# Performance work log

Measured on AMD Instinct MI355X. Metric: run time of the kernel, lower is better.

Reference implementation:

```python
import jax, jax.numpy as jnp
import numpy as np

HEADS = 4
EPS_LN = 1e-5
EPS_NORM = 1e-12

def conv1x1(x, w):
    # x: [B,C,T,H,W], w: [O,C] (Conv3d kernel_size=1, no bias)
    return jnp.einsum('oc,bcthw->bothw', w, x)

def dwconv3(x, w):
    # depthwise Conv3d 3x3x3, padding=1; w: [C,1,3,3,3]
    return jax.lax.conv_general_dilated(
        x, w, window_strides=(1, 1, 1), padding='SAME',
        dimension_numbers=('NCDHW', 'OIDHW', 'NCDHW'),
        feature_group_count=x.shape[1])

def layernorm_c(x, w, b):
    # LayerNorm over channel dim (torch LN applied after b c t h w -> b (thw) c)
    m = jnp.mean(x, axis=1, keepdims=True)
    v = jnp.mean(jnp.square(x - m), axis=1, keepdims=True)
    xn = (x - m) * jax.lax.rsqrt(v + EPS_LN)
    return xn * w[None, :, None, None, None] + b[None, :, None, None, None]

def l2norm(x):
    n = jnp.sqrt(jnp.sum(jnp.square(x), axis=-1, keepdims=True))
    return x / jnp.maximum(n, EPS_NORM)

def attention_c(x, qkv_w, qkv_dw_w, proj_w, temperature):
    B, C, T, H, W = x.shape
    qkv = dwconv3(conv1x1(x, qkv_w), qkv_dw_w)  # [B,3C,T,H,W]
    q, k, v = jnp.split(qkv, 3, axis=1)
    def to_heads(a):
        return a.reshape(B, HEADS, C // HEADS, T * H * W)  # b head c (thw)
    q, k, v = to_heads(q), to_heads(k), to_heads(v)
    q = l2norm(q)
    k = l2norm(k)
    # channel attention: [b,h,c,c] score matrix scaled by learnable temperature
    attn = jnp.einsum('bhcn,bhdn->bhcd', q, k) * temperature[None]
    attn = jax.nn.softmax(attn, axis=-1)
    out = jnp.einsum('bhcd,bhdn->bhcn', attn, v)
    out = out.reshape(B, C, T, H, W)
    return conv1x1(out, proj_w)

def feedforward(x, pin_w, ffn_dw_w, pout_w):
    h = conv1x1(x, pin_w)            # [B,2H,T,H,W]
    h = dwconv3(h, ffn_dw_w)
    x1, x2 = jnp.split(h, 2, axis=1)
    g = jax.nn.gelu(x1, approximate=False) * x2
    return conv1x1(g, pout_w)

def setup_inputs() -> dict:
    key = jax.random.key(0)
    ks = jax.random.split(key, 8)
    C, T, H, W = 192, 10, 64, 64
    Hf = int(C * 2.66)  # 510
    s = 0.05
    return {
        'x': jax.random.normal(ks[0], (1, C, T, H, W), jnp.float32),
        'ln1_w': jnp.ones((C,), jnp.float32),
        'ln1_b': jnp.zeros((C,), jnp.float32),
        'qkv_w': jax.random.normal(ks[1], (3 * C, C), jnp.float32) * s,
        'qkv_dw_w': jax.random.normal(ks[2], (3 * C, 1, 3, 3, 3), jnp.float32) * s,
        'proj_w': jax.random.normal(ks[3], (C, C), jnp.float32) * s,
        'temperature': jnp.ones((HEADS, 1, 1), jnp.float32),
        'ln2_w': jnp.ones((C,), jnp.float32),
        'ln2_b': jnp.zeros((C,), jnp.float32),
        'pin_w': jax.random.normal(ks[4], (2 * Hf, C), jnp.float32) * s,
        'ffn_dw_w': jax.random.normal(ks[5], (2 * Hf, 1, 3, 3, 3), jnp.float32) * s,
        'pout_w': jax.random.normal(ks[6], (C, Hf), jnp.float32) * s,
    }

def reference(x, ln1_w, ln1_b, qkv_w, qkv_dw_w, proj_w, temperature,
              ln2_w, ln2_b, pin_w, ffn_dw_w, pout_w):
    y = x + attention_c(layernorm_c(x, ln1_w, ln1_b), qkv_w, qkv_dw_w, proj_w, temperature)
    out = y + feedforward(layernorm_c(y, ln2_w, ln2_b), pin_w, ffn_dw_w, pout_w)
    return out
```

## Files before the change

### kernel.cpp

```cpp
#include <hip/hip_runtime.h>
#include <math.h>

#define NPOS 40960
#define TT 10
#define HH 64
#define WW 64
#define HWP 4096
#define CIN 192
#define C3 576
#define NHEADS 4
#define CHD 48
#define HF 510
#define GNB 80
#define GCHUNK 512

typedef unsigned short u16;
typedef unsigned int   u32;
typedef __bf16 bf16x8 __attribute__((ext_vector_type(8)));
typedef __bf16 bf16x2 __attribute__((ext_vector_type(2)));
typedef float  f32x4  __attribute__((ext_vector_type(4)));
typedef u16    u16x8  __attribute__((ext_vector_type(8)));
typedef u32    u32x4  __attribute__((ext_vector_type(4)));

__device__ __forceinline__ float b2f(u16 u) {
    return __uint_as_float(((unsigned int)u) << 16);
}
__device__ __forceinline__ u16 f2b(float f) {
    unsigned int i = __float_as_uint(f);
    unsigned int r = (i + 0x7FFFu + ((i >> 16) & 1u)) >> 16;
    return (u16)r;
}
__device__ __forceinline__ u16 f2bh(float f) {
    return __builtin_bit_cast(u16, static_cast<__bf16>(f));
}
__device__ __forceinline__ float gelu_exact(float v) {
    return 0.5f * v * (1.0f + erff(v * 0.70710678118654752f));
}
__device__ __forceinline__ float gelu_fast(float v) {
    float z = fabsf(v) * 0.70710678118654752f;
    float d = fmaf(0.3275911f, z, 1.0f);
#if __has_builtin(__builtin_amdgcn_rcpf)
    float t = __builtin_amdgcn_rcpf(d);
#else
    float t = 1.0f / d;
#endif
    float p = fmaf(1.061405429f, t, -1.453152027f);
    p = fmaf(p, t, 1.421413741f);
    p = fmaf(p, t, -0.284496736f);
    p = fmaf(p, t, 0.254829592f);
    p = p * t;
    float e = __expf(-z * z);
    float E = fmaf(-p, e, 1.0f);
    return 0.5f * v * (1.0f + copysignf(E, v));
}

__device__ __forceinline__ float dot2bf(u32 a, u32 b, float c) {
#if __has_builtin(__builtin_amdgcn_fdot2_f32_bf16)
    return __builtin_amdgcn_fdot2_f32_bf16(
        __builtin_bit_cast(bf16x2, a), __builtin_bit_cast(bf16x2, b), c, false);
#else
    float a0 = b2f((u16)(a & 0xffffu)), a1 = b2f((u16)(a >> 16));
    float b0 = b2f((u16)(b & 0xffffu)), b1 = b2f((u16)(b >> 16));
    return fmaf(a1, b1, fmaf(a0, b0, c));
#endif
}
__device__ __forceinline__ u32 alignp(u32 hi, u32 lo) {
#if __has_builtin(__builtin_amdgcn_alignbit)
    return __builtin_amdgcn_alignbit(hi, lo, 16);
#else
    return (lo >> 16) | (hi << 16);
#endif
}

__device__ __forceinline__ u32 dpp_prev(u32 v) {
#if __has_builtin(__builtin_amdgcn_update_dpp)
    return (u32)__builtin_amdgcn_update_dpp(0, (int)v, 0x111, 0xF, 0xF, true);
#else
    return __shfl(v, (threadIdx.x & 63) - 1);
#endif
}
__device__ __forceinline__ u32 dpp_next(u32 v) {
#if __has_builtin(__builtin_amdgcn_update_dpp)
    return (u32)__builtin_amdgcn_update_dpp(0, (int)v, 0x101, 0xF, 0xF, true);
#else
    return __shfl(v, (threadIdx.x & 63) + 1);
#endif
}

#define GLD_LDS16(g, l) __builtin_amdgcn_global_load_lds( \
    (const __attribute__((address_space(1))) void*)(g), \
    (__attribute__((address_space(3))) void*)(l), 16, 0, 0)

#define CVT_N1 (640 * 192)
#define CVT_N2 (1024 * 192)
#define CVT_N3 (256 * 512)
__global__ void cvtw_k(const float* __restrict__ qkv_w, const float* __restrict__ pin_w,
                       const float* __restrict__ pout_w,
                       u16* __restrict__ qkv_wb, u16* __restrict__ pin_wb,
                       u16* __restrict__ pout_wb) {
    int idx = blockIdx.x * 256 + threadIdx.x;
    if (idx < CVT_N1) {
        int r = idx / 192, c = idx % 192;
        qkv_wb[idx] = f2bh(r < 576 ? qkv_w[r * 192 + c] : 0.f);
    } else if (idx < CVT_N1 + CVT_N2) {
        int k = idx - CVT_N1;
        int r = k / 192, c = k % 192;
        pin_wb[k] = f2bh(r < 1020 ? pin_w[r * 192 + c] : 0.f);
    } else if (idx < CVT_N1 + CVT_N2 + CVT_N3) {
        int k = idx - CVT_N1 - CVT_N2;
        int r = k / 512, c = k % 512;
        pout_wb[k] = f2bh((r < 192 && c < 510) ? pout_w[r * 510 + c] : 0.f);
    }
}

template<typename InT>
__global__ __launch_bounds__(256) void lnt_k(const InT* __restrict__ X,
                                             const float* __restrict__ w,
                                             const float* __restrict__ b,
                                             u16* __restrict__ Xt) {
    __shared__ float sm[CIN][65];
    __shared__ float ps[4][64], ps2[4][64];
    __shared__ float smean[64], srstd[64];
    __shared__ float sw[CIN], sb[CIN];
    const int tid = threadIdx.x;
    const int n0 = blockIdx.x * 64;
    if (tid < CIN) { sw[tid] = w[tid]; sb[tid] = b[tid]; }
    if constexpr (sizeof(InT) == 4) {
        #pragma unroll
        for (int i = 0; i < 12; ++i) {
            int e = i * 256 + tid;
            int c = e >> 4, p4 = (e & 15) * 4;
            float4 v = *(const float4*)((const float*)X + (size_t)c * NPOS + n0 + p4);
            sm[c][p4 + 0] = v.x; sm[c][p4 + 1] = v.y;
            sm[c][p4 + 2] = v.z; sm[c][p4 + 3] = v.w;
        }
    } else {
        #pragma unroll
        for (int i = 0; i < 6; ++i) {
            int e = i * 256 + tid;
            int c = e >> 3, p8 = (e & 7) * 8;
            u16x8 v = *(const u16x8*)((const u16*)X + (size_t)c * NPOS + n0 + p8);
            #pragma unroll
            for (int j = 0; j < 8; ++j) sm[c][p8 + j] = b2f(v[j]);
        }
    }
    __syncthreads();
    int g = tid >> 6, nn = tid & 63;
    float s = 0.f, s2 = 0.f;
    for (int c = g * 48; c < g * 48 + 48; ++c) {
        float v = sm[c][nn];
        s += v; s2 += v * v;
    }
    ps[g][nn] = s; ps2[g][nn] = s2;
    __syncthreads();
    if (g == 0) {
        float t = ps[0][nn] + ps[1][nn] + ps[2][nn] + ps[3][nn];
        float t2 = ps2[0][nn] + ps2[1][nn] + ps2[2][nn] + ps2[3][nn];
        float m = t / CIN;
        float var = t2 / CIN - m * m;
        smean[nn] = m;
        srstd[nn] = rsqrtf(var + 1e-5f);
    }
    __syncthreads();
    #pragma unroll
    for (int i = 0; i < 6; ++i) {
        int e = i * 256 + tid;
        int nl = e / 24, cg = e % 24;
        int c0 = cg * 8;
        float m = smean[nl], rs_ = srstd[nl];
        u16x8 o;
        #pragma unroll
        for (int j = 0; j < 8; ++j) {
            float v = (sm[c0 + j][nl] - m) * rs_ * sw[c0 + j] + sb[c0 + j];
            o[j] = f2bh(v);
        }
        *(u16x8*)(Xt + (size_t)(n0 + nl) * CIN + c0) = o;
    }
}

__global__ __launch_bounds__(256) void transpose_pad_k(const u16* __restrict__ src,
                                                       u16* __restrict__ dst,
                                                       int CS, int CD) {
    __shared__ float sm[64][65];
    const int tid = threadIdx.x;
    const int n0 = blockIdx.x * 64;
    const int cb = blockIdx.y * 64;
    #pragma unroll
    for (int i = 0; i < 2; ++i) {
        int e = i * 256 + tid;
        int cl = e >> 3, nn8 = (e & 7) * 8;
        int c = cb + cl;
        if (c < CS) {
            u16x8 v = *(const u16x8*)(src + (size_t)c * NPOS + n0 + nn8);
            #pragma unroll
            for (int j = 0; j < 8; ++j) sm[cl][nn8 + j] = b2f(v[j]);
        } else {
            #pragma unroll
            for (int j = 0; j < 8; ++j) sm[cl][nn8 + j] = 0.f;
        }
    }
    __syncthreads();
    #pragma unroll
    for (int i = 0; i < 2; ++i) {
        int e = i * 256 + tid;
        int nl = e >> 3, c0 = (e & 7) * 8;
        u16x8 o;
        #pragma unroll
        for (int j = 0; j < 8; ++j) o[j] = f2bh(sm[c0 + j][nl]);
        *(u16x8*)(dst + (size_t)(n0 + nl) * CD + cb + c0) = o;
    }
}

template<int KP, typename OutT, typename ResT, bool RESID>
__global__ __launch_bounds__(256) void gemm_mfma_k(
    const u16* __restrict__ A, const u16* __restrict__ Bt, int O,
    const ResT* __restrict__ resid, OutT* __restrict__ outp)
{
    constexpr int NT = KP / 32;
    __shared__ u16 As[2][128 * 32];
    __shared__ u16 Bs[2][128 * 32];
    const int tid  = threadIdx.x;
    const int lane = tid & 63;
    const int wv   = tid >> 6;
    const int lo = lane & 15, hi = lane >> 4;
    const int m_blk = blockIdx.y * 128;
    const int n_blk = blockIdx.x * 128;

    int bb0 = (0 * 4 + wv) * 1024 + lane * 16;
    int bb1 = (1 * 4 + wv) * 1024 + lane * 16;
    const int r0 = bb0 >> 6, c80 = (bb0 >> 4) & 3;
    const int r1 = bb1 >> 6, c81 = (bb1 >> 4) & 3;

    auto stage = [&](int buf, int k0) {
        GLD_LDS16(A  + (size_t)(m_blk + r0) * KP + k0 + c80 * 8, (char*)&As[buf][0] + (0 * 4 + wv) * 1024);
        GLD_LDS16(A  + (size_t)(m_blk + r1) * KP + k0 + c81 * 8, (char*)&As[buf][0] + (1 * 4 + wv) * 1024);
        GLD_LDS16(Bt + (size_t)(n_blk + r0) * KP + k0 + c80 * 8, (char*)&Bs[buf][0] + (0 * 4 + wv) * 1024);
        GLD_LDS16(Bt + (size_t)(n_blk + r1) * KP + k0 + c81 * 8, (char*)&Bs[buf][0] + (1 * 4 + wv) * 1024);
    };

    f32x4 acc[4][4];
    const f32x4 zero = {0.f, 0.f, 0.f, 0.f};
    #pragma unroll
    for (int mt = 0; mt < 4; ++mt)
        #pragma unroll
        for (int nt = 0; nt < 4; ++nt) acc[mt][nt] = zero;

    stage(0, 0);
    __syncthreads();

    #pragma unroll
    for (int t = 0; t < NT; ++t) {
        if (t + 1 < NT) stage((t + 1) & 1, (t + 1) * 32);
        const u16* Ab = &As[t & 1][0] + (wv & 1) * 64 * 32;
        const u16* Bb = &Bs[t & 1][0] + (wv >> 1) * 64 * 32;
        bf16x8 a[4], b[4];
        #pragma unroll
        for (int q = 0; q < 4; ++q) {
            a[q] = *(const bf16x8*)(Ab + (q * 16 + lo) * 32 + hi * 8);
            b[q] = *(const bf16x8*)(Bb + (q * 16 + lo) * 32 + hi * 8);
        }
        #pragma unroll
        for (int mt = 0; mt < 4; ++mt)
            #pragma unroll
            for (int nt = 0; nt < 4; ++nt)
                acc[mt][nt] = __builtin_amdgcn_mfma_f32_16x16x32_bf16(
                    a[mt], b[nt], acc[mt][nt], 0, 0, 0);
        __syncthreads();
    }

    const int m_base = m_blk + (wv & 1) * 64;
    const int n_base = n_blk + (wv >> 1) * 64;
    #pragma unroll
    for (int mt = 0; mt < 4; ++mt) {
        #pragma unroll
        for (int r = 0; r < 4; ++r) {
            int m = m_base + mt * 16 + hi * 4 + r;
            if (m < O) {
                size_t rowoff = (size_t)m * NPOS;
                #pragma unroll
                for (int nt = 0; nt < 4; ++nt) {
                    int n = n_base + nt * 16 + lo;
                    float v = acc[mt][nt][r];
                    if (RESID) {
                        if constexpr (sizeof(ResT) == 2) v += b2f(((const u16*)resid)[rowoff + n]);
                        else                             v += ((const float*)resid)[rowoff + n];
                    }
                    if constexpr (sizeof(OutT) == 2) outp[rowoff + n] = (OutT)f2bh(v);
                    else                             outp[rowoff + n] = (OutT)v;
                }
            }
        }
    }
}

__global__ __launch_bounds__(256) void dwconv_k(const u16* __restrict__ in,
                                                u16* __restrict__ outp,
                                                const float* __restrict__ wgt,
                                                float* __restrict__ nrm2)
{
    __shared__ float red[256];
    const int lane = threadIdx.x & 63;
    const int wv   = threadIdx.x >> 6;
    const int c    = blockIdx.x >> 1;
    const int hb   = blockIdx.x & 1;
    const int h    = hb * 32 + wv * 8 + (lane >> 3);
    const int w0c  = (lane & 7) * 8;
    const bool wl0 = (lane & 7) == 0;
    const bool wl7 = (lane & 7) == 7;
    const bool hup = (h > 0), hdn = (h < HH - 1);
    u32 W01[9], W2h[9];
    {
        const float* wc = wgt + c * 27;
        #pragma unroll
        for (int i = 0; i < 9; ++i) {
            float a = wc[i * 3 + 0], b = wc[i * 3 + 1], d = wc[i * 3 + 2];
            W01[i] = (u32)f2b(a) | ((u32)f2b(b) << 16);
            W2h[i] = ((u32)f2b(d)) << 16;
        }
    }
    const u16* base = in   + (size_t)c * (TT * HWP);
    u16*       ob   = outp + (size_t)c * (TT * HWP);

    u32x4 zv = {0u, 0u, 0u, 0u};
    u32x4 ld[3][3];
    auto issue = [&](int ph, int ts) {
        const u16* rp = base + (size_t)ts * HWP + h * WW + w0c;
        ld[ph][0] = hup ? *(const u32x4*)(rp - WW) : zv;
        ld[ph][1] = *(const u32x4*)(rp);
        ld[ph][2] = hdn ? *(const u32x4*)(rp + WW) : zv;
    };

    float acc[3][8];
    #pragma unroll
    for (int o_ = 0; o_ < 3; ++o_)
        #pragma unroll
        for (int j = 0; j < 8; ++j) acc[o_][j] = 0.f;
    float sq = 0.f;

    issue(0, 0);
    issue(1, 1);
    #pragma unroll
    for (int ts = 0; ts < TT; ++ts) {
        const int cb = ts % 3;
        if (ts + 2 < TT) issue((ts + 2) % 3, ts + 2);
        #pragma unroll
        for (int dh = 0; dh < 3; ++dh) {
            u32 P0 = ld[cb][dh][0], P1 = ld[cb][dh][1];
            u32 P2 = ld[cb][dh][2], P3 = ld[cb][dh][3];
            u32 Pm = dpp_prev(P3); Pm = wl0 ? 0u : Pm;
            u32 Pp = dpp_next(P0); Pp = wl7 ? 0u : Pp;
            u32 S0 = alignp(P0, Pm), S1 = alignp(P1, P0);
            u32 S2 = alignp(P2, P1), S3 = alignp(P3, P2);
            u32 S4 = alignp(Pp, P3);
            #pragma unroll
            for (int tp = 0; tp < 3; ++tp) {
                int o_;
                if (tp == 2) { if (ts < 1) continue; o_ = (ts - 1) % 3; }
                else if (tp == 1) { o_ = ts % 3; }
                else { if (ts + 1 >= TT) continue; o_ = (ts + 1) % 3; }
                const u32 wA = W01[tp * 3 + dh], wB = W2h[tp * 3 + dh];
                float* ap = acc[o_];
                ap[0] = dot2bf(S0, wA, ap[0]); ap[0] = dot2bf(P0, wB, ap[0]);
                ap[1] = dot2bf(P0, wA, ap[1]); ap[1] = dot2bf(S1, wB, ap[1]);
                ap[2] = dot2bf(S1, wA, ap[2]); ap[2] = dot2bf(P1, wB, ap[2]);
                ap[3] = dot2bf(P1, wA, ap[3]); ap[3] = dot2bf(S2, wB, ap[3]);
                ap[4] = dot2bf(S2, wA, ap[4]); ap[4] = dot2bf(P2, wB, ap[4]);
                ap[5] = dot2bf(P2, wA, ap[5]); ap[5] = dot2bf(S3, wB, ap[5]);
                ap[6] = dot2bf(S3, wA, ap[6]); ap[6] = dot2bf(P3, wB, ap[6]);
                ap[7] = dot2bf(P3, wA, ap[7]); ap[7] = dot2bf(S4, wB, ap[7]);
            }
        }
        if (ts >= 1) {
            const int o_ = (ts - 1) % 3;
            u16x8 o;
            #pragma unroll
            for (int j = 0; j < 8; ++j) {
                float v = acc[o_][j];
                sq = fmaf(v, v, sq);
                o[j] = f2bh(v);
            }
            *(u16x8*)(ob + (size_t)(ts - 1) * HWP + h * WW + w0c) = o;
            #pragma unroll
            for (int j = 0; j < 8; ++j) acc[o_][j] = 0.f;
        }
    }
    {
        const int o_ = (TT - 1) % 3;
        u16x8 o;
        #pragma unroll
        for (int j = 0; j < 8; ++j) {
            float v = acc[o_][j];
            sq = fmaf(v, v, sq);
            o[j] = f2bh(v);
        }
        *(u16x8*)(ob + (size_t)(TT - 1) * HWP + h * WW + w0c) = o;
    }
    if (nrm2) {
        red[threadIdx.x] = sq;
        __syncthreads();
        for (int off = 128; off > 0; off >>= 1) {
            if (threadIdx.x < off) red[threadIdx.x] += red[threadIdx.x + off];
            __syncthreads();
        }
        if (threadIdx.x == 0) nrm2[c * 2 + hb] = red[0];
    }
}

__global__ __launch_bounds__(256) void dwconv_glu2_k(const u16* __restrict__ in,
                                                     u16* __restrict__ gout,
                                                     const float* __restrict__ wgt)
{
    __shared__ float gbuf[2][16][66];
    const int tid  = threadIdx.x;
    const int lane = tid & 63;
    const int wv   = tid >> 6;
    const int ch   = wv >> 1;
    const int wvc  = wv & 1;
    const int cpr  = blockIdx.x >> 2;
    const int hb   = blockIdx.x & 3;
    const int hr   = wvc * 8 + (lane >> 3);
    const int h    = hb * 16 + hr;
    const int w0c  = (lane & 7) * 8;
    const bool wl0 = (lane & 7) == 0;
    const bool wl7 = (lane & 7) == 7;
    const bool hup = (h > 0), hdn = (h < HH - 1);

    const int cc = __builtin_amdgcn_readfirstlane(cpr + ch * HF);
    u32 W01[9], W2h[9];
    {
        const float* wc = wgt + (size_t)cc * 27;
        #pragma unroll
        for (int i = 0; i < 9; ++i) {
            float a = wc[i * 3 + 0], b = wc[i * 3 + 1], d = wc[i * 3 + 2];
            W01[i] = (u32)f2b(a) | ((u32)f2b(b) << 16);
            W2h[i] = ((u32)f2b(d)) << 16;
        }
    }
    const u16* base = in + (size_t)cc * (TT * HWP);
    u16* ob = gout + (size_t)cpr * (TT * HWP);

    u32x4 zv = {0u, 0u, 0u, 0u};
    u32x4 ld[3][3];
    auto issue = [&](int ph, int ts) {
        const u16* rp = base + (size_t)ts * HWP + h * WW + w0c;
        ld[ph][0] = hup ? *(const u32x4*)(rp - WW) : zv;
        ld[ph][1] = *(const u32x4*)(rp);
        ld[ph][2] = hdn ? *(const u32x4*)(rp + WW) : zv;
    };

    float acc[3][8];
    #pragma unroll
    for (int o_ = 0; o_ < 3; ++o_)
        #pragma unroll
        for (int j = 0; j < 8; ++j) acc[o_][j] = 0.f;

    auto emit = [&](int ots) {
        const int o_ = ots % 3;
        const int bf = ots & 1;
        if (ch == 0) {
            #pragma unroll
            for (int j = 0; j < 8; ++j) {
                float a = acc[o_][j];
                gbuf[bf][hr][w0c + j] = (j < 4) ? gelu_fast(a) : a;
            }
        }
        __syncthreads();
        if (ch == 1) {
            u16x8 o;
            #pragma unroll
            for (int j = 0; j < 8; ++j) {
                float v = gbuf[bf][hr][w0c + j];
                float g = (j < 4) ? v : gelu_fast(v);
                o[j] = f2bh(g * acc[o_][j]);
            }
            *(u16x8*)(ob + (size_t)ots * HWP + h * WW + w0c) = o;
        }
        #pragma unroll
        for (int j = 0; j < 8; ++j) acc[o_][j] = 0.f;
    };

    issue(0, 0);
    issue(1, 1);
    #pragma unroll
    for (int ts = 0; ts < TT; ++ts) {
        const int cb = ts % 3;
        if (ts + 2 < TT) issue((ts + 2) % 3, ts + 2);
        #pragma unroll
        for (int dh = 0; dh < 3; ++dh) {
            u32 P0 = ld[cb][dh][0], P1 = ld[cb][dh][1];
            u32 P2 = ld[cb][dh][2], P3 = ld[cb][dh][3];
            u32 Pm = dpp_prev(P3); Pm = wl0 ? 0u : Pm;
            u32 Pp = dpp_next(P0); Pp = wl7 ? 0u : Pp;
            u32 S0 = alignp(P0, Pm), S1 = alignp(P1, P0);
            u32 S2 = alignp(P2, P1), S3 = alignp(P3, P2);
            u32 S4 = alignp(Pp, P3);
            #pragma unroll
            for (int tp = 0; tp < 3; ++tp) {
                int o_;
                if (tp == 2) { if (ts < 1) continue; o_ = (ts - 1) % 3; }
                else if (tp == 1) { o_ = ts % 3; }
                else { if (ts + 1 >= TT) continue; o_ = (ts + 1) % 3; }
                const u32 wA = W01[tp * 3 + dh], wB = W2h[tp * 3 + dh];
                float* ap = acc[o_];
                ap[0] = dot2bf(S0, wA, ap[0]); ap[0] = dot2bf(P0, wB, ap[0]);
                ap[1] = dot2bf(P0, wA, ap[1]); ap[1] = dot2bf(S1, wB, ap[1]);
                ap[2] = dot2bf(S1, wA, ap[2]); ap[2] = dot2bf(P1, wB, ap[2]);
                ap[3] = dot2bf(P1, wA, ap[3]); ap[3] = dot2bf(S2, wB, ap[3]);
                ap[4] = dot2bf(S2, wA, ap[4]); ap[4] = dot2bf(P2, wB, ap[4]);
                ap[5] = dot2bf(P2, wA, ap[5]); ap[5] = dot2bf(S3, wB, ap[5]);
                ap[6] = dot2bf(S3, wA, ap[6]); ap[6] = dot2bf(P3, wB, ap[6]);
                ap[7] = dot2bf(P3, wA, ap[7]); ap[7] = dot2bf(S4, wB, ap[7]);
            }
        }
        if (ts >= 1) emit(ts - 1);
    }
    emit(TT - 1);
}

__global__ __launch_bounds__(64) void gram_k(const u16* __restrict__ qkv,
                                             float* __restrict__ part) {
    const int h  = blockIdx.x / GNB;
    const int nb = blockIdx.x % GNB;
    const int lane = threadIdx.x;
    const int lo = lane & 15, hi = lane >> 4;
    const u16* qp = qkv + (size_t)(h * CHD) * NPOS + (size_t)nb * GCHUNK + hi * 8;
    const u16* kp = qkv + (size_t)(CIN + h * CHD) * NPOS + (size_t)nb * GCHUNK + hi * 8;
    f32x4 acc[3][3];
    const f32x4 zero = {0.f, 0.f, 0.f, 0.f};
    #pragma unroll
    for (int mt = 0; mt < 3; ++mt)
        #pragma unroll
        for (int nt = 0; nt < 3; ++nt) acc[mt][nt] = zero;
    #pragma unroll
    for (int ks = 0; ks < GCHUNK; ks += 32) {
        bf16x8 a[3], b[3];
        #pragma unroll
        for (int t = 0; t < 3; ++t) {
            a[t] = *(const bf16x8*)(qp + (size_t)(t * 16 + lo) * NPOS + ks);
            b[t] = *(const bf16x8*)(kp + (size_t)(t * 16 + lo) * NPOS + ks);
        }
        #pragma unroll
        for (int mt = 0; mt < 3; ++mt)
            #pragma unroll
            for (int nt = 0; nt < 3; ++nt)
                acc[mt][nt] = __builtin_amdgcn_mfma_f32_16x16x32_bf16(
                    a[mt], b[nt], acc[mt][nt], 0, 0, 0);
    }
    float* pp = part + (size_t)blockIdx.x * 2304;
    #pragma unroll
    for (int mt = 0; mt < 3; ++mt)
        #pragma unroll
        for (int nt = 0; nt < 3; ++nt)
            #pragma unroll
            for (int r = 0; r < 4; ++r)
                pp[(mt * 16 + hi * 4 + r) * 48 + nt * 16 + lo] = acc[mt][nt][r];
}

__global__ __launch_bounds__(64) void gram_softmax_k(const float* __restrict__ part,
                                                     const float* __restrict__ norm2p,
                                                     const float* __restrict__ temp,
                                                     float* __restrict__ attn) {
    const int row = blockIdx.x;
    const int h = row / CHD, r = row % CHD;
    const int d = threadIdx.x;
    float s = 0.f;
    if (d < CHD) {
        const float* pp = part + (size_t)h * GNB * 2304 + r * 48 + d;
        for (int nb = 0; nb < GNB; ++nb) s += pp[(size_t)nb * 2304];
    }
    float v = -1e30f;
    if (d < CHD) {
        float qn = fmaxf(sqrtf(norm2p[2 * row] + norm2p[2 * row + 1]), 1e-12f);
        int kc = CIN + h * CHD + d;
        float kn = fmaxf(sqrtf(norm2p[2 * kc] + norm2p[2 * kc + 1]), 1e-12f);
        v = temp[h] * s / (qn * kn);
    }
    float mx = v;
    #pragma unroll
    for (int o = 32; o > 0; o >>= 1) mx = fmaxf(mx, __shfl_xor(mx, o));
    float e = (d < CHD) ? expf(v - mx) : 0.f;
    float se = e;
    #pragma unroll
    for (int o = 32; o > 0; o >>= 1) se += __shfl_xor(se, o);
    if (d < CHD) attn[row * CHD + d] = e / se;
}

__global__ void mmat_k(const float* __restrict__ proj_w, const float* __restrict__ attn,
                       u16* __restrict__ Mb) {
    int idx = blockIdx.x * blockDim.x + threadIdx.x;
    if (idx >= 256 * CIN) return;
    int o = idx / CIN, j = idx % CIN;
    float s = 0.f;
    if (o < CIN) {
        int h = j / CHD, d = j % CHD;
        for (int c = 0; c < CHD; ++c)
            s += proj_w[o * CIN + h * CHD + c] * attn[(h * CHD + c) * CHD + d];
    }
    Mb[idx] = f2bh(s);
}

extern "C" void kernel_launch(void* const* d_in, const int* in_sizes, int n_in,
                              void* d_out, int out_size, void* d_ws, size_t ws_size,
                              hipStream_t stream) {
    const float* x       = (const float*)d_in[0];
    const float* ln1w    = (const float*)d_in[1];
    const float* ln1b    = (const float*)d_in[2];
    const float* qkv_w   = (const float*)d_in[3];
    const float* qkv_dw  = (const float*)d_in[4];
    const float* proj_w  = (const float*)d_in[5];
    const float* temp    = (const float*)d_in[6];
    const float* ln2w    = (const float*)d_in[7];
    const float* ln2b    = (const float*)d_in[8];
    const float* pin_w   = (const float*)d_in[9];
    const float* ffn_dw  = (const float*)d_in[10];
    const float* pout_w  = (const float*)d_in[11];
    float* out = (float*)d_out;

    char* wsb = (char*)d_ws;
    size_t off = 0;
    auto alloc = [&](size_t bytes) {
        void* p = wsb + off; off += (bytes + 255) & ~(size_t)255; return p;
    };
    float* norm2p  = (float*)alloc(C3 * 2 * 4);
    float* attn    = (float*)alloc(NHEADS * 2304 * 4);
    float* part    = (float*)alloc((size_t)NHEADS * GNB * 2304 * 4);
    u16*   qkv_wb  = (u16*)alloc((size_t)640 * 192 * 2);
    u16*   pin_wb  = (u16*)alloc((size_t)1024 * 192 * 2);
    u16*   pout_wb = (u16*)alloc((size_t)256 * 512 * 2);
    u16*   M_b     = (u16*)alloc((size_t)256 * 192 * 2);
    u16*   xn1_t   = (u16*)alloc((size_t)NPOS * 192 * 2);
    u16*   yn2_t   = (u16*)alloc((size_t)NPOS * 192 * 2);
    u16*   ybuf    = (u16*)alloc((size_t)CIN * NPOS * 2);
    u16*   regionA = (u16*)alloc((size_t)1024 * NPOS * 2);
    u16*   regionB = (u16*)alloc((size_t)1024 * NPOS * 2);
    u16* qkv_raw  = regionA;
    u16* qkv_conv = regionB;
    u16* h_raw    = regionA;
    u16* g510     = regionB;
    u16* gt       = regionA;
    u16* vt       = xn1_t;

    cvtw_k<<<(CVT_N1 + CVT_N2 + CVT_N3 + 255) / 256, 256, 0, stream>>>(
        qkv_w, pin_w, pout_w, qkv_wb, pin_wb, pout_wb);
    lnt_k<float><<<NPOS / 64, 256, 0, stream>>>(x, ln1w, ln1b, xn1_t);
    gemm_mfma_k<192, u16, float, false><<<dim3(NPOS / 128, 5), 256, 0, stream>>>(
        qkv_wb, xn1_t, C3, nullptr, qkv_raw);
    dwconv_k<<<C3 * 2, 256, 0, stream>>>(qkv_raw, qkv_conv, qkv_dw, norm2p);
    gram_k<<<NHEADS * GNB, 64, 0, stream>>>(qkv_conv, part);
    gram_softmax_k<<<192, 64, 0, stream>>>(part, norm2p, temp, attn);
    mmat_k<<<(256 * CIN + 255) / 256, 256, 0, stream>>>(proj_w, attn, M_b);
    transpose_pad_k<<<dim3(NPOS / 64, 3), 256, 0, stream>>>(
        qkv_conv + (size_t)384 * NPOS, vt, 192, 192);
    gemm_mfma_k<192, u16, float, true><<<dim3(NPOS / 128, 2), 256, 0, stream>>>(
        M_b, vt, CIN, x, ybuf);
    lnt_k<u16><<<NPOS / 64, 256, 0, stream>>>(ybuf, ln2w, ln2b, yn2_t);
    gemm_mfma_k<192, u16, float, false><<<dim3(NPOS / 128, 8), 256, 0, stream>>>(
        pin_wb, yn2_t, 1024, nullptr, h_raw);
    dwconv_glu2_k<<<HF * 4, 256, 0, stream>>>(h_raw, g510, ffn_dw);
    transpose_pad_k<<<dim3(NPOS / 64, 8), 256, 0, stream>>>(g510, gt, HF, 512);
    gemm_mfma_k<512, float, u16, true><<<dim3(NPOS / 128, 2), 256, 0, stream>>>(
        pout_wb, gt, CIN, ybuf, out);
}
```

Measured before the change: 232.8 us.

## Compute both GLU channels per thread to remove LDS exchange and barriers

New measurement: 233.6 us. Within noise of the previous version (+0.4%).

```diff
diff --git a/kernel.cpp b/kernel.cpp
--- a/kernel.cpp
+++ b/kernel.cpp
@@ -20,7 +20,9 @@
 typedef __bf16 bf16x2 __attribute__((ext_vector_type(2)));
 typedef float  f32x4  __attribute__((ext_vector_type(4)));
 typedef u16    u16x8  __attribute__((ext_vector_type(8)));
+typedef u16    u16x4  __attribute__((ext_vector_type(4)));
 typedef u32    u32x4  __attribute__((ext_vector_type(4)));
+typedef u32    u32x2  __attribute__((ext_vector_type(2)));
 
 __device__ __forceinline__ float b2f(u16 u) {
     return __uint_as_float(((unsigned int)u) << 16);
@@ -32,9 +34,6 @@
 }
 __device__ __forceinline__ u16 f2bh(float f) {
     return __builtin_bit_cast(u16, static_cast<__bf16>(f));
-}
-__device__ __forceinline__ float gelu_exact(float v) {
-    return 0.5f * v * (1.0f + erff(v * 0.70710678118654752f));
 }
 __device__ __forceinline__ float gelu_fast(float v) {
     float z = fabsf(v) * 0.70710678118654752f;
@@ -76,15 +75,27 @@
 #if __has_builtin(__builtin_amdgcn_update_dpp)
     return (u32)__builtin_amdgcn_update_dpp(0, (int)v, 0x111, 0xF, 0xF, true);
 #else
-    return __shfl(v, (threadIdx.x & 63) - 1);
+    int l = (int)(threadIdx.x & 63);
+    u32 r = __shfl(v, l - 1);
+    return ((l & 15) == 0) ? 0u : r;
 #endif
 }
 __device__ __forceinline__ u32 dpp_next(u32 v) {
 #if __has_builtin(__builtin_amdgcn_update_dpp)
     return (u32)__builtin_amdgcn_update_dpp(0, (int)v, 0x101, 0xF, 0xF, true);
 #else
-    return __shfl(v, (threadIdx.x & 63) + 1);
+    int l = (int)(threadIdx.x & 63);
+    u32 r = __shfl(v, l + 1);
+    return ((l & 15) == 15) ? 0u : r;
 #endif
+}
+__device__ __forceinline__ u32 dpp_prev8(u32 v, bool edge) {
+    u32 r = dpp_prev(v);
+    return edge ? 0u : r;
+}
+__device__ __forceinline__ u32 dpp_next8(u32 v, bool edge) {
+    u32 r = dpp_next(v);
+    return edge ? 0u : r;
 }
 
 #define GLD_LDS16(g, l) __builtin_amdgcn_global_load_lds( \
@@ -347,8 +358,8 @@
         for (int dh = 0; dh < 3; ++dh) {
             u32 P0 = ld[cb][dh][0], P1 = ld[cb][dh][1];
             u32 P2 = ld[cb][dh][2], P3 = ld[cb][dh][3];
-            u32 Pm = dpp_prev(P3); Pm = wl0 ? 0u : Pm;
-            u32 Pp = dpp_next(P0); Pp = wl7 ? 0u : Pp;
+            u32 Pm = dpp_prev8(P3, wl0);
+            u32 Pp = dpp_next8(P0, wl7);
             u32 S0 = alignp(P0, Pm), S1 = alignp(P1, P0);
             u32 S2 = alignp(P2, P1), S3 = alignp(P3, P2);
             u32 S4 = alignp(Pp, P3);
@@ -406,77 +417,63 @@
     }
 }
 
-__global__ __launch_bounds__(256) void dwconv_glu2_k(const u16* __restrict__ in,
+__global__ __launch_bounds__(256) void dwconv_glu3_k(const u16* __restrict__ in,
                                                      u16* __restrict__ gout,
                                                      const float* __restrict__ wgt)
 {
-    __shared__ float gbuf[2][16][66];
-    const int tid  = threadIdx.x;
-    const int lane = tid & 63;
-    const int wv   = tid >> 6;
-    const int ch   = wv >> 1;
-    const int wvc  = wv & 1;
+    const int lane = threadIdx.x & 63;
+    const int wv   = threadIdx.x >> 6;
     const int cpr  = blockIdx.x >> 2;
     const int hb   = blockIdx.x & 3;
-    const int hr   = wvc * 8 + (lane >> 3);
-    const int h    = hb * 16 + hr;
-    const int w0c  = (lane & 7) * 8;
-    const bool wl0 = (lane & 7) == 0;
-    const bool wl7 = (lane & 7) == 7;
+    const int h    = hb * 16 + wv * 4 + (lane >> 4);
+    const int w0c  = (lane & 15) * 4;
     const bool hup = (h > 0), hdn = (h < HH - 1);
 
-    const int cc = __builtin_amdgcn_readfirstlane(cpr + ch * HF);
-    u32 W01[9], W2h[9];
-    {
-        const float* wc = wgt + (size_t)cc * 27;
+    u32 W01[2][9], W2h[2][9];
+    #pragma unroll
+    for (int ch = 0; ch < 2; ++ch) {
+        const float* wc = wgt + (size_t)(cpr + ch * HF) * 27;
         #pragma unroll
         for (int i = 0; i < 9; ++i) {
             float a = wc[i * 3 + 0], b = wc[i * 3 + 1], d = wc[i * 3 + 2];
-            W01[i] = (u32)f2b(a) | ((u32)f2b(b) << 16);
-            W2h[i] = ((u32)f2b(d)) << 16;
-        }
-    }
-    const u16* base = in + (size_t)cc * (TT * HWP);
+            W01[ch][i] = (u32)f2b(a) | ((u32)f2b(b) << 16);
+            W2h[ch][i] = ((u32)f2b(d)) << 16;
+        }
+    }
+    const u16* base0 = in + (size_t)cpr * (TT * HWP);
+    const u16* base1 = in + (size_t)(cpr + HF) * (TT * HWP);
     u16* ob = gout + (size_t)cpr * (TT * HWP);
 
-    u32x4 zv = {0u, 0u, 0u, 0u};
-    u32x4 ld[3][3];
+    u32x2 zv = {0u, 0u};
+    u32x2 ld[2][3][3];
     auto issue = [&](int ph, int ts) {
-        const u16* rp = base + (size_t)ts * HWP + h * WW + w0c;
-        ld[ph][0] = hup ? *(const u32x4*)(rp - WW) : zv;
-        ld[ph][1] = *(const u32x4*)(rp);
-        ld[ph][2] = hdn ? *(const u32x4*)(rp + WW) : zv;
+        const u16* rp0 = base0 + (size_t)ts * HWP + h * WW + w0c;
+        ld[0][ph][0] = hup ? *(const u32x2*)(rp0 - WW) : zv;
+        ld[0][ph][1] = *(const u32x2*)(rp0);
+        ld[0][ph][2] = hdn ? *(const u32x2*)(rp0 + WW) : zv;
+        const u16* rp1 = base1 + (size_t)ts * HWP + h * WW + w0c;
+        ld[1][ph][0] = hup ? *(const u32x2*)(rp1 - WW) : zv;
+        ld[1][ph][1] = *(const u32x2*)(rp1);
+        ld[1][ph][2] = hdn ? *(const u32x2*)(rp1 + WW) : zv;
     };
 
-    float acc[3][8];
-    #pragma unroll
-    for (int o_ = 0; o_ < 3; ++o_)
-        #pragma unroll
-        for (int j = 0; j < 8; ++j) acc[o_][j] = 0.f;
+    float acc[2][3][4];
+    #pragma unroll
+    for (int ch = 0; ch < 2; ++ch)
+        #pragma unroll
+        for (int o_ = 0; o_ < 3; ++o_)
+            #pragma unroll
+            for (int j = 0; j < 4; ++j) acc[ch][o_][j] = 0.f;
 
     auto emit = [&](int ots) {
         const int o_ = ots % 3;
-        const int bf = ots & 1;
-        if (ch == 0) {
-            #pragma unroll
-            for (int j = 0; j < 8; ++j) {
-                float a = acc[o_][j];
-                gbuf[bf][hr][w0c + j] = (j < 4) ? gelu_fast(a) : a;
-            }
-        }
-        __syncthreads();
-        if (ch == 1) {
-            u16x8 o;
-            #pragma unroll
-            for (int j = 0; j < 8; ++j) {
-                float v = gbuf[bf][hr][w0c + j];
-                float g = (j < 4) ? v : gelu_fast(v);
-                o[j] = f2bh(g * acc[o_][j]);
-            }
-            *(u16x8*)(ob + (size_t)ots * HWP + h * WW + w0c) = o;
-        }
-        #pragma unroll
-        for (int j = 0; j < 8; ++j) acc[o_][j] = 0.f;
+        u16x4 o;
+        #pragma unroll
+        for (int j = 0; j < 4; ++j)
+            o[j] = f2bh(gelu_fast(acc[0][o_][j]) * acc[1][o_][j]);
+        *(u16x4*)(ob + (size_t)ots * HWP + h * WW + w0c) = o;
+        #pragma unroll
+        for (int j = 0; j < 4; ++j) { acc[0][o_][j] = 0.f; acc[1][o_][j] = 0.f; }
     };
 
     issue(0, 0);
@@ -486,30 +483,26 @@
         const int cb = ts % 3;
         if (ts + 2 < TT) issue((ts + 2) % 3, ts + 2);
         #pragma unroll
-        for (int dh = 0; dh < 3; ++dh) {
-            u32 P0 = ld[cb][dh][0], P1 = ld[cb][dh][1];
-            u32 P2 = ld[cb][dh][2], P3 = ld[cb][dh][3];
-            u32 Pm = dpp_prev(P3); Pm = wl0 ? 0u : Pm;
-            u32 Pp = dpp_next(P0); Pp = wl7 ? 0u : Pp;
-            u32 S0 = alignp(P0, Pm), S1 = alignp(P1, P0);
-            u32 S2 = alignp(P2, P1), S3 = alignp(P3, P2);
-            u32 S4 = alignp(Pp, P3);
-            #pragma unroll
-            for (int tp = 0; tp < 3; ++tp) {
-                int o_;
-                if (tp == 2) { if (ts < 1) continue; o_ = (ts - 1) % 3; }
-                else if (tp == 1) { o_ = ts % 3; }
-                else { if (ts + 1 >= TT) continue; o_ = (ts + 1) % 3; }
-                const u32 wA = W01[tp * 3 + dh], wB = W2h[tp * 3 + dh];
-                float* ap = acc[o_];
-                ap[0] = dot2bf(S0, wA, ap[0]); ap[0] = dot2bf(P0, wB, ap[0]);
-                ap[1] = dot2bf(P0, wA, ap[1]); ap[1] = dot2bf(S1, wB, ap[1]);
-                ap[2] = dot2bf(S1, wA, ap[2]); ap[2] = dot2bf(P1, wB, ap[2]);
-                ap[3] = dot2bf(P1, wA, ap[3]); ap[3] = dot2bf(S2, wB, ap[3]);
-                ap[4] = dot2bf(S2, wA, ap[4]); ap[4] = dot2bf(P2, wB, ap[4]);
-                ap[5] = dot2bf(P2, wA, ap[5]); ap[5] = dot2bf(S3, wB, ap[5]);
-                ap[6] = dot2bf(S3, wA, ap[6]); ap[6] = dot2bf(P3, wB, ap[6]);
-                ap[7] = dot2bf(P3, wA, ap[7]); ap[7] = dot2bf(S4, wB, ap[7]);
+        for (int ch = 0; ch < 2; ++ch) {
+            #pragma unroll
+            for (int dh = 0; dh < 3; ++dh) {
+                u32 P0 = ld[ch][cb][dh][0], P1 = ld[ch][cb][dh][1];
+                u32 Pm = dpp_prev(P1);
+                u32 Pp = dpp_next(P0);
+                u32 S0 = alignp(P0, Pm), S1 = alignp(P1, P0), S2 = alignp(Pp, P1);
+                #pragma unroll
+                for (int tp = 0; tp < 3; ++tp) {
+                    int o_;
+                    if (tp == 2) { if (ts < 1) continue; o_ = (ts - 1) % 3; }
+                    else if (tp == 1) { o_ = ts % 3; }
+                    else { if (ts + 1 >= TT) continue; o_ = (ts + 1) % 3; }
+                    const u32 wA = W01[ch][tp * 3 + dh], wB = W2h[ch][tp * 3 + dh];
+                    float* ap = acc[ch][o_];
+                    ap[0] = dot2bf(S0, wA, ap[0]); ap[0] = dot2bf(P0, wB, ap[0]);
+                    ap[1] = dot2bf(P0, wA, ap[1]); ap[1] = dot2bf(S1, wB, ap[1]);
+                    ap[2] = dot2bf(S1, wA, ap[2]); ap[2] = dot2bf(P1, wB, ap[2]);
+                    ap[3] = dot2bf(P1, wA, ap[3]); ap[3] = dot2bf(S2, wB, ap[3]);
+                }
             }
         }
         if (ts >= 1) emit(ts - 1);
@@ -656,7 +649,7 @@
     lnt_k<u16><<<NPOS / 64, 256, 0, stream>>>(ybuf, ln2w, ln2b, yn2_t);
     gemm_mfma_k<192, u16, float, false><<<dim3(NPOS / 128, 8), 256, 0, stream>>>(
         pin_wb, yn2_t, 1024, nullptr, h_raw);
-    dwconv_glu2_k<<<HF * 4, 256, 0, stream>>>(h_raw, g510, ffn_dw);
+    dwconv_glu3_k<<<HF * 4, 256, 0, stream>>>(h_raw, g510, ffn_dw);
     transpose_pad_k<<<dim3(NPOS / 64, 8), 256, 0, stream>>>(g510, gt, HF, 512);
     gemm_mfma_k<512, float, u16, true><<<dim3(NPOS / 128, 2), 256, 0, stream>>>(
         pout_wb, gt, CIN, ybuf, out);
```
